# Kernel tuning notes

Hardware: AMD Instinct MI355X
Metric: run time of the kernel (lower is better)

The kernel has to match this reference:

```python
import jax, jax.numpy as jnp
import numpy as np

N_NODES = 50000
D_IN = 128
D_OUT = 64
N_ETYPES = 3
E_PER_ETYPE = 500000
P_ETYPE = 0.5  # self.p[etype] init value for every etype


def setup_inputs() -> dict:
    key = jax.random.key(0)
    k1, k2, k3, k4 = jax.random.split(key, 4)
    feat = jax.random.normal(k1, (N_NODES, D_IN), dtype=jnp.float32)
    W = jax.random.normal(k2, (D_IN, D_OUT), dtype=jnp.float32) * 0.05
    b = jax.random.normal(k3, (D_OUT,), dtype=jnp.float32) * 0.05
    # edge_index[e] = (src, dst) for etype e
    edge_index = jax.random.randint(k4, (N_ETYPES, 2, E_PER_ETYPE), 0, N_NODES, dtype=jnp.int64)
    return {"feat": feat, "W": W, "b": b, "edge_index": edge_index}


def reference(feat, W, b, edge_index):
    N = feat.shape[0]

    def agg_one_etype(ei):
        src, dst = ei[0], ei[1]
        # scatter-mean of src features onto dst nodes (dgl copy_u + mean)
        msg_sum = jax.ops.segment_sum(feat[src], dst, num_segments=N)          # [N, D]
        cnt = jax.ops.segment_sum(jnp.ones(src.shape, feat.dtype), dst, num_segments=N)
        hr = msg_sum / jnp.maximum(cnt, 1.0)[:, None]  # zero-in-degree nodes -> 0
        return jnp.tanh(hr)  # per-etype activation

    hr_all = jax.vmap(agg_one_etype)(edge_index)        # [n_etypes, N, D]
    h_homo = jnp.sum(hr_all * P_ETYPE, axis=0) + feat   # weighted sum + residual
    h_homo = jnp.tanh(h_homo)
    return h_homo @ W + b                               # final linear
```

## Files before the change

kernel.cpp:

```cpp
#include <hip/hip_runtime.h>
#include <hip/hip_bf16.h>

#define N_NODES 50000
#define D_IN 128
#define D_OUT 64
#define N_ETYPES 3
#define E_PER_ETYPE 500000
#define N_EDGES (N_ETYPES * E_PER_ETYPE)
#define CAP1 16
#define CAP2 30
#define NB_FEAT ((N_NODES * D_IN / 4) / 256)
#define NB_W ((D_IN * D_OUT) / 256)
#define CHUNK_EDGES 2048
#define N_CHUNKS ((N_EDGES + CHUNK_EDGES - 1) / CHUNK_EDGES)

typedef __attribute__((ext_vector_type(8))) short short8;
typedef __attribute__((ext_vector_type(4))) float f32x4;

static __device__ __forceinline__ unsigned short f2bf(float f) {
    unsigned int x = __float_as_uint(f);
    unsigned int lsb = (x >> 16) & 1u;
    x += 0x7fffu + lsb;
    return (unsigned short)(x >> 16);
}

static __device__ __forceinline__ float fast_tanh(float x) {
    float e = __expf(2.0f * x);
    return 1.0f - 2.0f * __builtin_amdgcn_rcpf(e + 1.0f);
}

static __device__ __forceinline__ short8 as_s8(uint4 u) {
    union { uint4 u; short8 s; } cv; cv.u = u; return cv.s;
}

static __device__ __forceinline__ void accum8(float* ax, uint4 p) {
    ax[0] += __uint_as_float(p.x << 16);
    ax[1] += __uint_as_float(p.x & 0xffff0000u);
    ax[2] += __uint_as_float(p.y << 16);
    ax[3] += __uint_as_float(p.y & 0xffff0000u);
    ax[4] += __uint_as_float(p.z << 16);
    ax[5] += __uint_as_float(p.z & 0xffff0000u);
    ax[6] += __uint_as_float(p.w << 16);
    ax[7] += __uint_as_float(p.w & 0xffff0000u);
}

__global__ __launch_bounds__(256) void convert_kernel(
    const float* __restrict__ feat,
    unsigned short* __restrict__ featbf,
    const float* __restrict__ W,
    unsigned short* __restrict__ wtbf)
{
    int b = blockIdx.x;
    if (b < NB_FEAT) {
        int i = b * 256 + threadIdx.x;
        const float4* f4 = (const float4*)feat;
        float4 v = f4[i];
        ushort4 o;
        o.x = f2bf(v.x); o.y = f2bf(v.y); o.z = f2bf(v.z); o.w = f2bf(v.w);
        ((ushort4*)featbf)[i] = o;
    } else {
        int i = (b - NB_FEAT) * 256 + threadIdx.x;
        int n = i >> 7;
        int k = i & 127;
        wtbf[i] = f2bf(W[k * D_OUT + n]);
    }
}

__global__ __launch_bounds__(256) void fill_kernel(
    const int* __restrict__ edge_index,
    unsigned short* __restrict__ bucket1,
    unsigned short* __restrict__ spill,
    int* __restrict__ cnt)
{
    int slice = blockIdx.x & 7;
    int chunk = blockIdx.x >> 3;
    int e0 = chunk * CHUNK_EDGES + threadIdx.x;
    #pragma unroll
    for (int k = 0; k < CHUNK_EDGES / 256; k++) {
        int e = e0 + k * 256;
        if (e < N_EDGES) {
            int t  = e / E_PER_ETYPE;
            int ei = e - t * E_PER_ETYPE;
            const int* base = edge_index + (long long)t * 2 * E_PER_ETYPE;
            int dst = base[E_PER_ETYPE + ei];
            int s = (int)(((unsigned long long)(unsigned)dst * 687195ull) >> 32);
            if (s == slice) {
                int src = base[ei];
                int cell = t * N_NODES + dst;
                int pos = atomicAdd(cnt + cell, 1);
                if (pos < CAP1)
                    bucket1[(long long)cell * CAP1 + pos] = (unsigned short)src;
                else if (pos < CAP1 + CAP2)
                    spill[(long long)cell * CAP2 + (pos - CAP1)] = (unsigned short)src;
            }
        }
    }
}

__global__ __launch_bounds__(512) void gather_linear_kernel(
    const float* __restrict__ feat,
    const unsigned short* __restrict__ featbf,
    const unsigned short* __restrict__ wtbf,
    const float* __restrict__ bg,
    const unsigned short* __restrict__ bucket1,
    const unsigned short* __restrict__ spill,
    const int* __restrict__ cnt,
    float* __restrict__ out)
{
    __shared__ unsigned short hsb[16 * 128];

    int tid = threadIdx.x;
    ((unsigned int*)hsb)[512 + tid] = 0;

    int wave = tid >> 6;
    int lane = tid & 63;
    int sub  = lane >> 4;
    int sl   = lane & 15;
    int n = blockIdx.x * 8 + wave;

    int deg[N_ETYPES], idx[N_ETYPES];
    #pragma unroll
    for (int t = 0; t < N_ETYPES; t++) {
        int cell = t * N_NODES + n;
        int dg = cnt[cell];
        int id = 0;
        if (lane < CAP1) id = bucket1[(long long)cell * CAP1 + lane];
        else if (lane < CAP1 + CAP2 && dg > CAP1)
            id = spill[(long long)cell * CAP2 + (lane - CAP1)];
        deg[t] = dg; idx[t] = id;
    }

    const uint4* fb4 = (const uint4*)featbf;
    int k0 = 2 * sub;
    float s0 = 0.0f, s1 = 0.0f;

    #pragma unroll
    for (int t = 0; t < N_ETYPES; t++) {
        int d = (deg[t] < CAP1 + CAP2) ? deg[t] : (CAP1 + CAP2);
        float ax[8];
        #pragma unroll
        for (int k = 0; k < 8; k++) ax[k] = 0.0f;
        for (int j = 0; j < d; j += 8) {
            int ra = j + sub;
            int rb = j + 4 + sub;
            int ca = (ra < d - 1) ? ra : (d - 1);
            int cb = (rb < d - 1) ? rb : (d - 1);
            int sa = __shfl(idx[t], ca);
            int sb = __shfl(idx[t], cb);
            uint4 pa = fb4[(long long)sa * 16 + sl];
            uint4 pb = fb4[(long long)sb * 16 + sl];
            if (ra < d) accum8(ax, pa);
            if (rb < d) accum8(ax, pb);
        }
        #pragma unroll
        for (int k = 0; k < 8; k++) {
            ax[k] += __shfl_xor(ax[k], 16);
            ax[k] += __shfl_xor(ax[k], 32);
        }
        float inv = 1.0f / (float)((deg[t] > 0) ? deg[t] : 1);
        s0 += fast_tanh(ax[k0] * inv);
        s1 += fast_tanh(ax[k0 + 1] * inv);
    }

    float2 f = ((const float2*)feat)[(long long)n * 64 + (4 * sl + sub)];
    float hx = fast_tanh(f.x + 0.5f * s0);
    float hy = fast_tanh(f.y + 0.5f * s1);
    unsigned int hp = (unsigned int)f2bf(hx) | ((unsigned int)f2bf(hy) << 16);
    int wb = wave * 256 + ((16 * sl + 4 * sub) ^ (wave << 4));
    ((unsigned int*)hsb)[wb >> 2] = hp;

    uint4 b0 = {0,0,0,0}, b1 = {0,0,0,0}, b2 = {0,0,0,0}, b3 = {0,0,0,0};
    float bias = 0.0f;
    int sg = lane >> 4;
    if (wave < 4) {
        int nrow = wave * 16 + (lane & 15);
        const uint4* wt4 = (const uint4*)wtbf;
        b0 = wt4[nrow * 16 +  0 + sg];
        b1 = wt4[nrow * 16 +  4 + sg];
        b2 = wt4[nrow * 16 +  8 + sg];
        b3 = wt4[nrow * 16 + 12 + sg];
        bias = bg[nrow];
    }
    __syncthreads();

    if (wave < 4) {
        int row = lane & 15;
        int rbase = row * 256;
        int rx = (row & 7) << 4;
        const uint4* h4 = (const uint4*)hsb;
        uint4 a0 = h4[(rbase + (( 0 + sg * 16) ^ rx)) >> 4];
        uint4 a1 = h4[(rbase + (( 64 + sg * 16) ^ rx)) >> 4];
        uint4 a2 = h4[(rbase + ((128 + sg * 16) ^ rx)) >> 4];
        uint4 a3 = h4[(rbase + ((192 + sg * 16) ^ rx)) >> 4];

        f32x4 c = {bias, bias, bias, bias};
        c = __builtin_amdgcn_mfma_f32_16x16x32_bf16(as_s8(a0), as_s8(b0), c, 0, 0, 0);
        c = __builtin_amdgcn_mfma_f32_16x16x32_bf16(as_s8(a1), as_s8(b1), c, 0, 0, 0);
        c = __builtin_amdgcn_mfma_f32_16x16x32_bf16(as_s8(a2), as_s8(b2), c, 0, 0, 0);
        c = __builtin_amdgcn_mfma_f32_16x16x32_bf16(as_s8(a3), as_s8(b3), c, 0, 0, 0);

        #pragma unroll
        for (int i = 0; i < 4; i++) {
            int orow = sg * 4 + i;
            if (orow < 8)
                out[(long long)(blockIdx.x * 8 + orow) * 64 + wave * 16 + (lane & 15)] = c[i];
        }
    }
}

extern "C" void kernel_launch(void* const* d_in, const int* in_sizes, int n_in,
                              void* d_out, int out_size, void* d_ws, size_t ws_size,
                              hipStream_t stream) {
    const float* feat = (const float*)d_in[0];
    const float* W    = (const float*)d_in[1];
    const float* b    = (const float*)d_in[2];
    const int* edge_index = (const int*)d_in[3];
    float* out = (float*)d_out;

    size_t featbf_bytes  = (size_t)N_NODES * D_IN * sizeof(unsigned short);
    size_t bucket1_bytes = (size_t)N_ETYPES * N_NODES * CAP1 * sizeof(unsigned short);
    size_t spill_bytes   = (size_t)N_ETYPES * N_NODES * CAP2 * sizeof(unsigned short);
    size_t cnt_bytes     = (size_t)N_ETYPES * N_NODES * sizeof(int);
    size_t wtbf_bytes    = (size_t)D_IN * D_OUT * sizeof(unsigned short);
    if (ws_size < featbf_bytes + bucket1_bytes + spill_bytes + cnt_bytes + wtbf_bytes)
        return;

    unsigned short* featbf  = (unsigned short*)d_ws;
    unsigned short* bucket1 = (unsigned short*)((char*)d_ws + featbf_bytes);
    unsigned short* spill   = (unsigned short*)((char*)d_ws + featbf_bytes + bucket1_bytes);
    int* cnt = (int*)((char*)d_ws + featbf_bytes + bucket1_bytes + spill_bytes);
    unsigned short* wtbf = (unsigned short*)((char*)d_ws + featbf_bytes + bucket1_bytes
                                             + spill_bytes + cnt_bytes);

    hipMemsetAsync(cnt, 0, cnt_bytes, stream);

    convert_kernel<<<NB_FEAT + NB_W, 256, 0, stream>>>(feat, featbf, W, wtbf);

    fill_kernel<<<N_CHUNKS * 8, 256, 0, stream>>>(edge_index, bucket1, spill, cnt);

    gather_linear_kernel<<<N_NODES / 8, 512, 0, stream>>>(
        feat, featbf, wtbf, b, bucket1, spill, cnt, out);
}
```

Measured before the change: 216.9 us.

## Process two nodes per wave, pad with zero row, fold count reset into convert

The gather kernel now handles two destination nodes per wave (16 per block), so the MFMA tile is fully used and twice as many independent gather loads are in flight per lane. Out-of-range neighbor slots point at an appended all-zero feature row instead of being clamped and predicated. The cross-lane reduction becomes a reduce-scatter that needs fewer shuffles. The count buffer is zeroed inside the convert kernel rather than by a separate memset. The trade-offs are extra register pressure from the doubled accumulators and wasted loads when the two nodes have very different degrees.

```diff
diff --git a/kernel.cpp b/kernel.cpp
--- a/kernel.cpp
+++ b/kernel.cpp
@@ -9,8 +9,11 @@
 #define N_EDGES (N_ETYPES * E_PER_ETYPE)
 #define CAP1 16
 #define CAP2 30
+#define DMAX (CAP1 + CAP2)
+#define ZROW N_NODES
 #define NB_FEAT ((N_NODES * D_IN / 4) / 256)
 #define NB_W ((D_IN * D_OUT) / 256)
+#define NB_ZCNT 147
 #define CHUNK_EDGES 2048
 #define N_CHUNKS ((N_EDGES + CHUNK_EDGES - 1) / CHUNK_EDGES)
 
@@ -44,11 +47,31 @@
     ax[7] += __uint_as_float(p.w & 0xffff0000u);
 }
 
+static __device__ __forceinline__ float2 rs_reduce(const float* ax, int sub) {
+    bool hi = (sub & 1);
+    float k0_ = hi ? ax[4] : ax[0], s0_ = hi ? ax[0] : ax[4];
+    float k1_ = hi ? ax[5] : ax[1], s1_ = hi ? ax[1] : ax[5];
+    float k2_ = hi ? ax[6] : ax[2], s2_ = hi ? ax[2] : ax[6];
+    float k3_ = hi ? ax[7] : ax[3], s3_ = hi ? ax[3] : ax[7];
+    float h0 = k0_ + __shfl_xor(s0_, 16);
+    float h1 = k1_ + __shfl_xor(s1_, 16);
+    float h2 = k2_ + __shfl_xor(s2_, 16);
+    float h3 = k3_ + __shfl_xor(s3_, 16);
+    bool hi2 = (sub & 2);
+    float ka = hi2 ? h2 : h0, sa = hi2 ? h0 : h2;
+    float kb = hi2 ? h3 : h1, sb = hi2 ? h1 : h3;
+    float2 v;
+    v.x = ka + __shfl_xor(sa, 32);
+    v.y = kb + __shfl_xor(sb, 32);
+    return v;
+}
+
 __global__ __launch_bounds__(256) void convert_kernel(
     const float* __restrict__ feat,
     unsigned short* __restrict__ featbf,
     const float* __restrict__ W,
-    unsigned short* __restrict__ wtbf)
+    unsigned short* __restrict__ wtbf,
+    int* __restrict__ cnt)
 {
     int b = blockIdx.x;
     if (b < NB_FEAT) {
@@ -58,11 +81,20 @@
         ushort4 o;
         o.x = f2bf(v.x); o.y = f2bf(v.y); o.z = f2bf(v.z); o.w = f2bf(v.w);
         ((ushort4*)featbf)[i] = o;
-    } else {
+    } else if (b < NB_FEAT + NB_W) {
         int i = (b - NB_FEAT) * 256 + threadIdx.x;
         int n = i >> 7;
         int k = i & 127;
         wtbf[i] = f2bf(W[k * D_OUT + n]);
+    } else if (b == NB_FEAT + NB_W) {
+        if (threadIdx.x < 64)
+            ((unsigned int*)(featbf + (size_t)N_NODES * D_IN))[threadIdx.x] = 0;
+    } else {
+        int i = (b - NB_FEAT - NB_W - 1) * 256 + threadIdx.x;
+        if (i < (N_ETYPES * N_NODES) / 4) {
+            int4 z; z.x = 0; z.y = 0; z.z = 0; z.w = 0;
+            ((int4*)cnt)[i] = z;
+        }
     }
 }
 
@@ -89,9 +121,9 @@
                 int cell = t * N_NODES + dst;
                 int pos = atomicAdd(cnt + cell, 1);
                 if (pos < CAP1)
-                    bucket1[(long long)cell * CAP1 + pos] = (unsigned short)src;
+                    bucket1[cell * CAP1 + pos] = (unsigned short)src;
                 else if (pos < CAP1 + CAP2)
-                    spill[(long long)cell * CAP2 + (pos - CAP1)] = (unsigned short)src;
+                    spill[cell * CAP2 + (pos - CAP1)] = (unsigned short)src;
             }
         }
     }
@@ -110,88 +142,106 @@
     __shared__ unsigned short hsb[16 * 128];
 
     int tid = threadIdx.x;
-    ((unsigned int*)hsb)[512 + tid] = 0;
-
     int wave = tid >> 6;
     int lane = tid & 63;
     int sub  = lane >> 4;
     int sl   = lane & 15;
-    int n = blockIdx.x * 8 + wave;
-
-    int deg[N_ETYPES], idx[N_ETYPES];
+    int n0 = blockIdx.x * 16 + wave * 2;
+    int n1 = n0 + 1;
+
+    int degA[N_ETYPES], degB[N_ETYPES], idxA[N_ETYPES], idxB[N_ETYPES];
     #pragma unroll
     for (int t = 0; t < N_ETYPES; t++) {
-        int cell = t * N_NODES + n;
-        int dg = cnt[cell];
-        int id = 0;
-        if (lane < CAP1) id = bucket1[(long long)cell * CAP1 + lane];
-        else if (lane < CAP1 + CAP2 && dg > CAP1)
-            id = spill[(long long)cell * CAP2 + (lane - CAP1)];
-        deg[t] = dg; idx[t] = id;
-    }
+        int cell = t * N_NODES + n0;
+        int2 dg = *(const int2*)(cnt + cell);
+        int la = 0, lb = 0;
+        if (lane < CAP1) {
+            la = bucket1[cell * CAP1 + lane];
+            lb = bucket1[(cell + 1) * CAP1 + lane];
+        } else if (lane < DMAX) {
+            if (dg.x > CAP1) la = spill[cell * CAP2 + (lane - CAP1)];
+            if (dg.y > CAP1) lb = spill[(cell + 1) * CAP2 + (lane - CAP1)];
+        }
+        int ca = dg.x < DMAX ? dg.x : DMAX;
+        int cb = dg.y < DMAX ? dg.y : DMAX;
+        idxA[t] = (lane < ca) ? la : ZROW;
+        idxB[t] = (lane < cb) ? lb : ZROW;
+        degA[t] = dg.x; degB[t] = dg.y;
+    }
+
+    int k0 = ((sub & 1) << 2) | (sub & 2);
+    int p2 = 4 * sl + (k0 >> 1);
+    float2 fA = ((const float2*)feat)[n0 * 64 + p2];
+    float2 fB = ((const float2*)feat)[n1 * 64 + p2];
 
     const uint4* fb4 = (const uint4*)featbf;
-    int k0 = 2 * sub;
-    float s0 = 0.0f, s1 = 0.0f;
+    float s0A = 0.0f, s1A = 0.0f, s0B = 0.0f, s1B = 0.0f;
 
     #pragma unroll
     for (int t = 0; t < N_ETYPES; t++) {
-        int d = (deg[t] < CAP1 + CAP2) ? deg[t] : (CAP1 + CAP2);
-        float ax[8];
+        int da = degA[t] < DMAX ? degA[t] : DMAX;
+        int db = degB[t] < DMAX ? degB[t] : DMAX;
+        int dm = da > db ? da : db;
+        float axA[8], axB[8];
         #pragma unroll
-        for (int k = 0; k < 8; k++) ax[k] = 0.0f;
-        for (int j = 0; j < d; j += 8) {
-            int ra = j + sub;
-            int rb = j + 4 + sub;
-            int ca = (ra < d - 1) ? ra : (d - 1);
-            int cb = (rb < d - 1) ? rb : (d - 1);
-            int sa = __shfl(idx[t], ca);
-            int sb = __shfl(idx[t], cb);
-            uint4 pa = fb4[(long long)sa * 16 + sl];
-            uint4 pb = fb4[(long long)sb * 16 + sl];
-            if (ra < d) accum8(ax, pa);
-            if (rb < d) accum8(ax, pb);
-        }
-        #pragma unroll
-        for (int k = 0; k < 8; k++) {
-            ax[k] += __shfl_xor(ax[k], 16);
-            ax[k] += __shfl_xor(ax[k], 32);
-        }
-        float inv = 1.0f / (float)((deg[t] > 0) ? deg[t] : 1);
-        s0 += fast_tanh(ax[k0] * inv);
-        s1 += fast_tanh(ax[k0 + 1] * inv);
-    }
-
-    float2 f = ((const float2*)feat)[(long long)n * 64 + (4 * sl + sub)];
-    float hx = fast_tanh(f.x + 0.5f * s0);
-    float hy = fast_tanh(f.y + 0.5f * s1);
-    unsigned int hp = (unsigned int)f2bf(hx) | ((unsigned int)f2bf(hy) << 16);
-    int wb = wave * 256 + ((16 * sl + 4 * sub) ^ (wave << 4));
-    ((unsigned int*)hsb)[wb >> 2] = hp;
+        for (int k = 0; k < 8; k++) { axA[k] = 0.0f; axB[k] = 0.0f; }
+        for (int j = 0; j < dm; j += 8) {
+            int r0 = j + sub;
+            int r1 = j + 4 + sub;
+            int sa0 = __shfl(idxA[t], r0);
+            int sa1 = __shfl(idxA[t], r1);
+            int sb0 = __shfl(idxB[t], r0);
+            int sb1 = __shfl(idxB[t], r1);
+            uint4 pa0 = fb4[sa0 * 16 + sl];
+            uint4 pa1 = fb4[sa1 * 16 + sl];
+            uint4 pb0 = fb4[sb0 * 16 + sl];
+            uint4 pb1 = fb4[sb1 * 16 + sl];
+            accum8(axA, pa0); accum8(axA, pa1);
+            accum8(axB, pb0); accum8(axB, pb1);
+        }
+        float2 vA = rs_reduce(axA, sub);
+        float2 vB = rs_reduce(axB, sub);
+        float invA = __builtin_amdgcn_rcpf((float)(degA[t] > 0 ? degA[t] : 1));
+        float invB = __builtin_amdgcn_rcpf((float)(degB[t] > 0 ? degB[t] : 1));
+        s0A += fast_tanh(vA.x * invA);
+        s1A += fast_tanh(vA.y * invA);
+        s0B += fast_tanh(vB.x * invB);
+        s1B += fast_tanh(vB.y * invB);
+    }
+
+    float hxA = fast_tanh(fA.x + 0.5f * s0A);
+    float hyA = fast_tanh(fA.y + 0.5f * s1A);
+    float hxB = fast_tanh(fB.x + 0.5f * s0B);
+    float hyB = fast_tanh(fB.y + 0.5f * s1B);
+    unsigned int hpA = (unsigned int)f2bf(hxA) | ((unsigned int)f2bf(hyA) << 16);
+    unsigned int hpB = (unsigned int)f2bf(hxB) | ((unsigned int)f2bf(hyB) << 16);
+    int colb = 16 * sl + 2 * k0;
+    int rA = wave * 2, rB = rA + 1;
+    ((unsigned int*)hsb)[(rA * 256 + (colb ^ ((rA & 7) << 4))) >> 2] = hpA;
+    ((unsigned int*)hsb)[(rB * 256 + (colb ^ ((rB & 7) << 4))) >> 2] = hpB;
 
     uint4 b0 = {0,0,0,0}, b1 = {0,0,0,0}, b2 = {0,0,0,0}, b3 = {0,0,0,0};
     float bias = 0.0f;
-    int sg = lane >> 4;
     if (wave < 4) {
-        int nrow = wave * 16 + (lane & 15);
+        int nrow = wave * 16 + sl;
         const uint4* wt4 = (const uint4*)wtbf;
-        b0 = wt4[nrow * 16 +  0 + sg];
-        b1 = wt4[nrow * 16 +  4 + sg];
-        b2 = wt4[nrow * 16 +  8 + sg];
-        b3 = wt4[nrow * 16 + 12 + sg];
+        b0 = wt4[nrow * 16 +  0 + sub];
+        b1 = wt4[nrow * 16 +  4 + sub];
+        b2 = wt4[nrow * 16 +  8 + sub];
+        b3 = wt4[nrow * 16 + 12 + sub];
         bias = bg[nrow];
     }
     __syncthreads();
 
     if (wave < 4) {
-        int row = lane & 15;
+        int row = sl;
         int rbase = row * 256;
         int rx = (row & 7) << 4;
         const uint4* h4 = (const uint4*)hsb;
-        uint4 a0 = h4[(rbase + (( 0 + sg * 16) ^ rx)) >> 4];
-        uint4 a1 = h4[(rbase + (( 64 + sg * 16) ^ rx)) >> 4];
-        uint4 a2 = h4[(rbase + ((128 + sg * 16) ^ rx)) >> 4];
-        uint4 a3 = h4[(rbase + ((192 + sg * 16) ^ rx)) >> 4];
+        uint4 a0 = h4[(rbase + (( 0 + sub * 16) ^ rx)) >> 4];
+        uint4 a1 = h4[(rbase + (( 64 + sub * 16) ^ rx)) >> 4];
+        uint4 a2 = h4[(rbase + ((128 + sub * 16) ^ rx)) >> 4];
+        uint4 a3 = h4[(rbase + ((192 + sub * 16) ^ rx)) >> 4];
 
         f32x4 c = {bias, bias, bias, bias};
         c = __builtin_amdgcn_mfma_f32_16x16x32_bf16(as_s8(a0), as_s8(b0), c, 0, 0, 0);
@@ -201,9 +251,8 @@
 
         #pragma unroll
         for (int i = 0; i < 4; i++) {
-            int orow = sg * 4 + i;
-            if (orow < 8)
-                out[(long long)(blockIdx.x * 8 + orow) * 64 + wave * 16 + (lane & 15)] = c[i];
+            int orow = sub * 4 + i;
+            out[(blockIdx.x * 16 + orow) * 64 + wave * 16 + sl] = c[i];
         }
     }
 }
@@ -217,7 +266,7 @@
     const int* edge_index = (const int*)d_in[3];
     float* out = (float*)d_out;
 
-    size_t featbf_bytes  = (size_t)N_NODES * D_IN * sizeof(unsigned short);
+    size_t featbf_bytes  = (size_t)(N_NODES + 1) * D_IN * sizeof(unsigned short);
     size_t bucket1_bytes = (size_t)N_ETYPES * N_NODES * CAP1 * sizeof(unsigned short);
     size_t spill_bytes   = (size_t)N_ETYPES * N_NODES * CAP2 * sizeof(unsigned short);
     size_t cnt_bytes     = (size_t)N_ETYPES * N_NODES * sizeof(int);
@@ -232,12 +281,11 @@
     unsigned short* wtbf = (unsigned short*)((char*)d_ws + featbf_bytes + bucket1_bytes
                                              + spill_bytes + cnt_bytes);
 
-    hipMemsetAsync(cnt, 0, cnt_bytes, stream);
-
-    convert_kernel<<<NB_FEAT + NB_W, 256, 0, stream>>>(feat, featbf, W, wtbf);
+    convert_kernel<<<NB_FEAT + NB_W + 1 + NB_ZCNT, 256, 0, stream>>>(
+        feat, featbf, W, wtbf, cnt);
 
     fill_kernel<<<N_CHUNKS * 8, 256, 0, stream>>>(edge_index, bucket1, spill, cnt);
 
-    gather_linear_kernel<<<N_NODES / 8, 512, 0, stream>>>(
+    gather_linear_kernel<<<N_NODES / 16, 512, 0, stream>>>(
         feat, featbf, wtbf, b, bucket1, spill, cnt, out);
 }
```

Result: faster. 205.6 us (-5.2%).
